# Performance work log

Measured on AMD Instinct MI355X. Metric: run time of the kernel, lower is better.

## Reference

```python
import jax, jax.numpy as jnp
import numpy as np
from jax import lax

DT = 0.1


def setup_inputs() -> dict:
    key = jax.random.key(0)
    k1, k2, k3, k4 = jax.random.split(key, 4)
    Bsz, L, D, N, O = 32, 2048, 256, 64, 256
    x = jax.random.normal(k1, (Bsz, L, D), dtype=jnp.float32)
    # Shift A by 3*I so Re(eig(A)) > 0 -> bilinear-discretized A_tilde is stable
    A = jax.random.uniform(k2, (N, N), dtype=jnp.float32) + 3.0 * jnp.eye(N, dtype=jnp.float32)
    B = jax.random.uniform(k3, (N, D), dtype=jnp.float32)
    C = jax.random.uniform(k4, (O, N), dtype=jnp.float32)
    return {"x": x, "A": A, "B": B, "C": C}


def _s4_forward(x, A, B, C):
    N = A.shape[0]
    I = jnp.eye(N, dtype=A.dtype)
    # Bilinear discretization (as written in the torch source)
    tmp_inv = jnp.linalg.inv(I + A * (DT / 2))
    A_tilde = tmp_inv @ (I - A * (DT / 2))          # [N, N]
    B_tilde = (tmp_inv @ B) * DT                    # [N, D]

    L = x.shape[1]

    # K[i] = C @ A_tilde^i @ B_tilde; carry M = A_tilde^i @ B_tilde
    def step(M, _):
        return A_tilde @ M, C @ M                    # emit [O, D]

    _, K = lax.scan(step, B_tilde, None, length=L)   # K: [L, O, D]

    n = 2 * L - 1  # length after torch's F.pad(x, (0,0,0,L-1))
    x_fft = jnp.fft.rfft(x, n=n, axis=1)             # [B, F, D] complex
    K_fft = jnp.fft.rfft(K, n=n, axis=0)             # [F, O, D] complex
    y_fft = jnp.einsum('bfi,foi->bfo', x_fft, K_fft)
    y = jnp.fft.irfft(y_fft, n=n, axis=1)[:, :L]     # [B, L, O]
    return y


def reference(x, A, B, C):
    return _s4_forward(x, A, B, C)
```

## Files before the change

### kernel.cpp

```cpp
#include <hip/hip_runtime.h>

#define B_SZ   32
#define LEN    2048
#define DIM    256
#define NST    64
#define OUTD   256
#define CHUNK  64
#define NCHUNK (LEN / CHUNK)
#define ROWS   (B_SZ * LEN)

#define OFF_AT   0
#define OFF_A64  4096
#define OFF_CP   8192
#define OFF_S    24576
#define OFF_INST 90112
#define OFF_V    155648
#define OFF_H    OFF_V
#define WS_FLOATS (OFF_V + (size_t)ROWS * 64)

__device__ __forceinline__ void gload16(const float* gp, float* lds_base,
                                        int lane_off_f) {
#if __has_builtin(__builtin_amdgcn_global_load_lds)
  (void)lane_off_f;
  __builtin_amdgcn_global_load_lds(
      (const __attribute__((address_space(1))) unsigned int*)gp,
      (__attribute__((address_space(3))) unsigned int*)lds_base, 16, 0, 0);
#else
  float4 tmp = *(const float4*)gp;
  *(float4*)(lds_base + lane_off_f) = tmp;
#endif
}

__device__ __forceinline__ void mm64(float* dst, const float* a, const float* b,
                                     int t) {
  const int r0 = 4 * (t >> 4), c0 = 4 * (t & 15);
  float acc[4][4] = {};
  for (int k = 0; k < 64; ++k) {
    float4 bv = *(const float4*)(b + k * 68 + c0);
    for (int i = 0; i < 4; ++i) {
      float av = a[(r0 + i) * 68 + k];
      acc[i][0] = fmaf(av, bv.x, acc[i][0]);
      acc[i][1] = fmaf(av, bv.y, acc[i][1]);
      acc[i][2] = fmaf(av, bv.z, acc[i][2]);
      acc[i][3] = fmaf(av, bv.w, acc[i][3]);
    }
  }
  for (int i = 0; i < 4; ++i)
    *(float4*)(dst + (r0 + i) * 68 + c0) =
        make_float4(acc[i][0], acc[i][1], acc[i][2], acc[i][3]);
  __syncthreads();
}

__global__ __launch_bounds__(256) void k_fused0(const float* __restrict__ A,
                                                const float* __restrict__ Bm,
                                                const float* __restrict__ Cm,
                                                const float* __restrict__ x,
                                                float* __restrict__ ws) {
  __shared__ __align__(16) float sh[13056];
  const int t = threadIdx.x;

  if (blockIdx.x == 0) {
    float* Pa = sh;
    float* Pb = sh + 4352;
    float* Pc = sh + 8704;
    float* rbM = Pc;
    float* rbI = Pc + 128;
    float* cb  = Pc + 256;

    const int tc = t & 63;
    const int tr = t >> 6;
    float M[16], Iv[16];
    for (int i = 0; i < 16; ++i) {
      int r = 16 * tr + i;
      M[i] = 0.05f * A[r * 64 + tc] + (r == tc ? 1.0f : 0.0f);
      Iv[i] = (r == tc) ? 1.0f : 0.0f;
    }
    if (tr == 0) { rbM[tc] = M[0]; rbI[tc] = Iv[0]; }
    if (tc == 0)
      for (int i = 0; i < 16; ++i) cb[16 * tr + i] = M[i];
    __syncthreads();

#pragma unroll
    for (int k = 0; k < 64; ++k) {
      const int cur = (k & 1) * 64, nxt = ((k + 1) & 1) * 64;
      float rinv = 1.0f / rbM[cur + k];
      float rM = rbM[cur + tc] * rinv;
      float rI = rbI[cur + tc] * rinv;
#pragma unroll
      for (int i = 0; i < 16; ++i) {
        int r = 16 * tr + i;
        if (r == k) { M[i] = rM; Iv[i] = rI; }
        else {
          float f = cb[cur + r];
          M[i] = fmaf(-f, rM, M[i]);
          Iv[i] = fmaf(-f, rI, Iv[i]);
        }
      }
      if (k < 63) {
        if (tr == ((k + 1) >> 4)) {
          rbM[nxt + tc] = M[(k + 1) & 15];
          rbI[nxt + tc] = Iv[(k + 1) & 15];
        }
        if (tc == k + 1)
          for (int i = 0; i < 16; ++i) cb[nxt + 16 * tr + i] = M[i];
      }
      __syncthreads();
    }

    for (int i = 0; i < 16; ++i) {
      int r = 16 * tr + i;
      float at = 2.0f * Iv[i] - (r == tc ? 1.0f : 0.0f);
      ws[OFF_AT + r * 64 + tc] = at;
      Pa[r * 68 + tc] = at;
      Pc[r * 68 + tc] = Iv[i];
    }
    __syncthreads();

    mm64(Pb, Pa, Pa, t);
    mm64(Pa, Pb, Pb, t);
    mm64(Pb, Pa, Pa, t);
    mm64(Pa, Pb, Pb, t);
    mm64(Pb, Pa, Pa, t);
    mm64(Pa, Pb, Pb, t);
    for (int i = 0; i < 16; ++i) {
      int r = 16 * tr + i;
      ws[OFF_A64 + r * 64 + tc] = Pa[r * 68 + tc];
    }

    {
      const float* Crow = Cm + (size_t)t * 64;
      float4 acc4[16];
      for (int q = 0; q < 16; ++q) acc4[q] = make_float4(0.f, 0.f, 0.f, 0.f);
      for (int k = 0; k < 64; k += 4) {
        float4 c4 = *(const float4*)(Crow + k);
        float ck[4] = {c4.x, c4.y, c4.z, c4.w};
#pragma unroll
        for (int kk = 0; kk < 4; ++kk) {
          const float* mrow = Pc + (k + kk) * 68;
          float c = ck[kk];
#pragma unroll
          for (int q = 0; q < 16; ++q) {
            float4 mv = *(const float4*)(mrow + 4 * q);
            acc4[q].x = fmaf(c, mv.x, acc4[q].x);
            acc4[q].y = fmaf(c, mv.y, acc4[q].y);
            acc4[q].z = fmaf(c, mv.z, acc4[q].z);
            acc4[q].w = fmaf(c, mv.w, acc4[q].w);
          }
        }
      }
      float* cp = ws + OFF_CP + (size_t)t * 64;
      for (int q = 0; q < 16; ++q)
        *(float4*)(cp + 4 * q) =
            make_float4(0.1f * acc4[q].x, 0.1f * acc4[q].y, 0.1f * acc4[q].z,
                        0.1f * acc4[q].w);
    }
  } else {
    float* xs0 = sh;
    float* xs1 = sh + 4096;
    float* bs0 = sh + 8192;
    float* bs1 = sh + 10240;
    const int w = t >> 6, lane = t & 63;
    const int ro8 = lane >> 3, kq8 = lane & 7;
    const int rowbase = ((int)blockIdx.x - 1) * 128;

    auto stage = [&](int d0, float* xbuf, float* bbuf) {
#pragma unroll
      for (int c = 0; c < 4; ++c) {
        int q = 4 * w + c;
        const float* gp = x + (size_t)(rowbase + 8 * q + ro8) * 256 + d0 +
                          4 * (kq8 ^ (q & 7));
        gload16(gp, xbuf + q * 256, lane * 4);
      }
#pragma unroll
      for (int c = 0; c < 2; ++c) {
        int q = 2 * w + c;
        const float* gp =
            Bm + (size_t)(8 * q + ro8) * 256 + d0 + 4 * (kq8 ^ q);
        gload16(gp, bbuf + q * 256, lane * 4);
      }
    };

    stage(0, xs0, bs0);
    const int g = lane >> 4, lm = lane & 15;
    const int r0 = 32 * w + 8 * g, m0 = 4 * lm;
    const int ka = 4 * ((4 * w + g) & 7);
    const int kb = 4 * ((lm >> 1) & 7);
    float acc[8][4] = {};
    float* xc = xs0; float* xn = xs1; float* bc = bs0; float* bn = bs1;
    __syncthreads();

    for (int s = 0; s < 8; ++s) {
      if (s < 7) stage((s + 1) * 32, xn, bn);
      const float* xa = xc + r0 * 32;
      const float* bb = bc + m0 * 32;
#pragma unroll
      for (int k0 = 0; k0 < 32; k0 += 4) {
        float4 a4[8], b4[4];
#pragma unroll
        for (int i = 0; i < 8; ++i)
          a4[i] = *(const float4*)(xa + i * 32 + (k0 ^ ka));
#pragma unroll
        for (int j = 0; j < 4; ++j)
          b4[j] = *(const float4*)(bb + j * 32 + (k0 ^ kb));
#pragma unroll
        for (int i = 0; i < 8; ++i)
#pragma unroll
          for (int j = 0; j < 4; ++j) {
            acc[i][j] = fmaf(a4[i].x, b4[j].x, acc[i][j]);
            acc[i][j] = fmaf(a4[i].y, b4[j].y, acc[i][j]);
            acc[i][j] = fmaf(a4[i].z, b4[j].z, acc[i][j]);
            acc[i][j] = fmaf(a4[i].w, b4[j].w, acc[i][j]);
          }
      }
      __syncthreads();
      float* tp;
      tp = xc; xc = xn; xn = tp;
      tp = bc; bc = bn; bn = tp;
    }
    float* v = ws + OFF_V;
#pragma unroll
    for (int i = 0; i < 8; ++i)
      *(float4*)(v + (size_t)(rowbase + r0 + i) * 64 + m0) =
          make_float4(acc[i][0], acc[i][1], acc[i][2], acc[i][3]);
  }
}

__device__ __forceinline__ void load_areg(const float* __restrict__ M, int r,
                                          int q, float areg[16]) {
  const float4* ap = (const float4*)(M + r * 64 + q * 16);
  float4 a0 = ap[0], a1 = ap[1], a2 = ap[2], a3 = ap[3];
  areg[0] = a0.x; areg[1] = a0.y; areg[2] = a0.z; areg[3] = a0.w;
  areg[4] = a1.x; areg[5] = a1.y; areg[6] = a1.z; areg[7] = a1.w;
  areg[8] = a2.x; areg[9] = a2.y; areg[10] = a2.z; areg[11] = a2.w;
  areg[12] = a3.x; areg[13] = a3.y; areg[14] = a3.z; areg[15] = a3.w;
}

__device__ __forceinline__ float matvec_step(const float areg[16],
                                             const float* __restrict__ hcur,
                                             float* __restrict__ part, int r,
                                             int q, int t) {
  float4 ha = *(const float4*)(hcur + q * 16);
  float4 hb = *(const float4*)(hcur + q * 16 + 4);
  float4 hc = *(const float4*)(hcur + q * 16 + 8);
  float4 hd = *(const float4*)(hcur + q * 16 + 12);
  float p0 = fmaf(areg[0], ha.x, fmaf(areg[4], hb.x, fmaf(areg[8], hc.x, areg[12] * hd.x)));
  float p1 = fmaf(areg[1], ha.y, fmaf(areg[5], hb.y, fmaf(areg[9], hc.y, areg[13] * hd.y)));
  float p2 = fmaf(areg[2], ha.z, fmaf(areg[6], hb.z, fmaf(areg[10], hc.z, areg[14] * hd.z)));
  float p3 = fmaf(areg[3], ha.w, fmaf(areg[7], hb.w, fmaf(areg[11], hc.w, areg[15] * hd.w)));
  part[q * 68 + r] = (p0 + p1) + (p2 + p3);
  __syncthreads();
  float s = 0.0f;
  if (t < 64) s = part[t] + part[68 + t] + part[136 + t] + part[204 + t];
  return s;
}

__global__ __launch_bounds__(256) void k_chunk(float* __restrict__ ws, int phase) {
  __shared__ __align__(16) float hcur[64];
  __shared__ __align__(16) float part[4 * 68];
  __shared__ __align__(16) float ulds[CHUNK * 64];
  const int t = threadIdx.x;
  const int c = blockIdx.x, b = blockIdx.y;
  const int r = t & 63, q = t >> 6;
  float areg[16];
  load_areg(ws + OFF_AT, r, q, areg);
  const float* u = ws + OFF_V + (size_t)(b * LEN + c * CHUNK) * 64;
  for (int i = 0; i < 4; ++i) {
    int e = 4 * (t + 256 * i);
    *(float4*)(ulds + e) = *(const float4*)(u + e);
  }
  if (t < 64)
    hcur[t] = (phase == 3) ? ws[OFF_INST + (b * NCHUNK + c) * 64 + t] : 0.0f;
  __syncthreads();
  for (int st = 0; st < CHUNK; ++st) {
    float s = matvec_step(areg, hcur, part, r, q, t);
    if (t < 64) {
      float hn = s + ulds[st * 64 + t];
      hcur[t] = hn;
      if (phase == 3)
        ws[OFF_H + (size_t)(b * LEN + c * CHUNK + st) * 64 + t] = hn;
      else if (st == CHUNK - 1)
        ws[OFF_S + (b * NCHUNK + c) * 64 + t] = hn;
    }
    __syncthreads();
  }
}

__global__ __launch_bounds__(256) void k_carry(float* __restrict__ ws) {
  __shared__ __align__(16) float hcur[64];
  __shared__ __align__(16) float part[4 * 68];
  __shared__ __align__(16) float slds[NCHUNK * 64];
  const int t = threadIdx.x;
  const int b = blockIdx.x;
  const int r = t & 63, q = t >> 6;
  float areg[16];
  load_areg(ws + OFF_A64, r, q, areg);
  for (int i = 0; i < 2; ++i) {
    int e = 4 * (t + 256 * i);
    *(float4*)(slds + e) = *(const float4*)(ws + OFF_S + b * NCHUNK * 64 + e);
  }
  if (t < 64) {
    hcur[t] = 0.0f;
    ws[OFF_INST + (b * NCHUNK) * 64 + t] = 0.0f;
  }
  __syncthreads();
  for (int c = 1; c < NCHUNK; ++c) {
    float s = matvec_step(areg, hcur, part, r, q, t);
    if (t < 64) {
      float hn = s + slds[(c - 1) * 64 + t];
      hcur[t] = hn;
      ws[OFF_INST + (b * NCHUNK + c) * 64 + t] = hn;
    }
    __syncthreads();
  }
}

__global__ __launch_bounds__(256) void k_ygemm(const float* __restrict__ ws,
                                               float* __restrict__ y) {
  __shared__ __align__(16) float sh[16384];
  float* hs = sh;
  float* cs = sh + 8192;
  const int t = threadIdx.x;
  const int w = t >> 6, lane = t & 63;
  const int rowbase = blockIdx.x * 128;
  const int obase = blockIdx.y * 128;
  const float* H = ws + OFF_H;
  const float* CP = ws + OFF_CP;

  const int ro4 = lane >> 4, kq16 = lane & 15;
#pragma unroll
  for (int c = 0; c < 8; ++c) {
    int q = 8 * w + c;
    int row = 4 * q + ro4;
    int sd = 4 * (kq16 ^ ((row >> 3) & 7));
    gload16(H + (size_t)(rowbase + row) * 64 + sd, hs + q * 256, lane * 4);
    gload16(CP + (size_t)(obase + row) * 64 + sd, cs + q * 256, lane * 4);
  }
  __syncthreads();

  const int g = lane >> 4, lm = lane & 15;
  const int r0 = 32 * w + 8 * g, o0 = 8 * lm;
  const int ka = 4 * ((4 * w + g) & 7);
  const int kb = 4 * (lm & 7);
  const float* ha = hs + r0 * 64;
  const float* cbp = cs + o0 * 64;
  float acc[8][8] = {};
#pragma unroll
  for (int k0 = 0; k0 < 64; k0 += 4) {
    float4 a4[8], b4[8];
#pragma unroll
    for (int i = 0; i < 8; ++i)
      a4[i] = *(const float4*)(ha + i * 64 + (k0 ^ ka));
#pragma unroll
    for (int j = 0; j < 8; ++j)
      b4[j] = *(const float4*)(cbp + j * 64 + (k0 ^ kb));
#pragma unroll
    for (int i = 0; i < 8; ++i)
#pragma unroll
      for (int j = 0; j < 8; ++j) {
        acc[i][j] = fmaf(a4[i].x, b4[j].x, acc[i][j]);
        acc[i][j] = fmaf(a4[i].y, b4[j].y, acc[i][j]);
        acc[i][j] = fmaf(a4[i].z, b4[j].z, acc[i][j]);
        acc[i][j] = fmaf(a4[i].w, b4[j].w, acc[i][j]);
      }
  }
#pragma unroll
  for (int i = 0; i < 8; ++i) {
    float* yp = y + (size_t)(rowbase + r0 + i) * 256 + obase + o0;
    *(float4*)(yp) = make_float4(acc[i][0], acc[i][1], acc[i][2], acc[i][3]);
    *(float4*)(yp + 4) = make_float4(acc[i][4], acc[i][5], acc[i][6], acc[i][7]);
  }
}

extern "C" void kernel_launch(void* const* d_in, const int* in_sizes, int n_in,
                              void* d_out, int out_size, void* d_ws,
                              size_t ws_size, hipStream_t stream) {
  const float* x = (const float*)d_in[0];
  const float* A = (const float*)d_in[1];
  const float* Bm = (const float*)d_in[2];
  const float* Cm = (const float*)d_in[3];
  float* y = (float*)d_out;
  float* ws = (float*)d_ws;
  if (ws_size < (size_t)WS_FLOATS * sizeof(float)) return;

  hipLaunchKernelGGL(k_fused0, dim3(1 + ROWS / 128), dim3(256), 0, stream, A,
                     Bm, Cm, x, ws);
  hipLaunchKernelGGL(k_chunk, dim3(NCHUNK, B_SZ), dim3(256), 0, stream, ws, 1);
  hipLaunchKernelGGL(k_carry, dim3(B_SZ), dim3(256), 0, stream, ws);
  hipLaunchKernelGGL(k_chunk, dim3(NCHUNK, B_SZ), dim3(256), 0, stream, ws, 3);
  hipLaunchKernelGGL(k_ygemm, dim3(ROWS / 128, OUTD / 128), dim3(256), 0,
                     stream, ws, y);
}
```

Baseline: 260.3 us.

## Fuse y GEMM into chunk scan, one-wave-per-chunk recurrences, register-resident x GEMM

Replaces the four-wave matvec recurrence, which needed block-wide barriers every step, with one wavefront per chunk holding a full row of A_tilde in registers. The output GEMM against C' is fused into the second chunk pass, so the H state is never written to or re-read from global memory. The x·B GEMM now streams x directly into registers with B staged in LDS. The A^64 power and C' products move into extra blocks of the first chunk pass. Trade-offs: 64-float register arrays per thread, a large LDS footprint that limits occupancy, and dependence on the ordering of launches within one stream.

```diff
diff --git a/kernel.cpp b/kernel.cpp
--- a/kernel.cpp
+++ b/kernel.cpp
@@ -10,13 +10,15 @@
 #define ROWS   (B_SZ * LEN)
 
 #define OFF_AT   0
-#define OFF_A64  4096
-#define OFF_CP   8192
-#define OFF_S    24576
-#define OFF_INST 90112
-#define OFF_V    155648
-#define OFF_H    OFF_V
+#define OFF_P64  4096
+#define OFF_MINV 8192
+#define OFF_CP   12288
+#define OFF_S    28672
+#define OFF_INST 94208
+#define OFF_V    159744
 #define WS_FLOATS (OFF_V + (size_t)ROWS * 64)
+
+#define KEYR(row) ((((row) >> 3) ^ (row)) & 7)
 
 __device__ __forceinline__ void gload16(const float* gp, float* lds_base,
                                         int lane_off_f) {
@@ -37,6 +39,7 @@
   float acc[4][4] = {};
   for (int k = 0; k < 64; ++k) {
     float4 bv = *(const float4*)(b + k * 68 + c0);
+#pragma unroll
     for (int i = 0; i < 4; ++i) {
       float av = a[(r0 + i) * 68 + k];
       acc[i][0] = fmaf(av, bv.x, acc[i][0]);
@@ -45,6 +48,8 @@
       acc[i][3] = fmaf(av, bv.w, acc[i][3]);
     }
   }
+  __syncthreads();
+#pragma unroll
   for (int i = 0; i < 4; ++i)
     *(float4*)(dst + (r0 + i) * 68 + c0) =
         make_float4(acc[i][0], acc[i][1], acc[i][2], acc[i][3]);
@@ -53,23 +58,19 @@
 
 __global__ __launch_bounds__(256) void k_fused0(const float* __restrict__ A,
                                                 const float* __restrict__ Bm,
-                                                const float* __restrict__ Cm,
                                                 const float* __restrict__ x,
                                                 float* __restrict__ ws) {
-  __shared__ __align__(16) float sh[13056];
+  __shared__ __align__(16) float sh[16384];
   const int t = threadIdx.x;
 
   if (blockIdx.x == 0) {
-    float* Pa = sh;
-    float* Pb = sh + 4352;
-    float* Pc = sh + 8704;
-    float* rbM = Pc;
-    float* rbI = Pc + 128;
-    float* cb  = Pc + 256;
-
+    float* rbM = sh;
+    float* rbI = sh + 128;
+    float* cb  = sh + 256;
     const int tc = t & 63;
     const int tr = t >> 6;
     float M[16], Iv[16];
+#pragma unroll
     for (int i = 0; i < 16; ++i) {
       int r = 16 * tr + i;
       M[i] = 0.05f * A[r * 64 + tc] + (r == tc ? 1.0f : 0.0f);
@@ -79,7 +80,6 @@
     if (tc == 0)
       for (int i = 0; i < 16; ++i) cb[16 * tr + i] = M[i];
     __syncthreads();
-
 #pragma unroll
     for (int k = 0; k < 64; ++k) {
       const int cur = (k & 1) * 64, nxt = ((k + 1) & 1) * 64;
@@ -106,268 +106,297 @@
       }
       __syncthreads();
     }
-
+#pragma unroll
     for (int i = 0; i < 16; ++i) {
       int r = 16 * tr + i;
-      float at = 2.0f * Iv[i] - (r == tc ? 1.0f : 0.0f);
-      ws[OFF_AT + r * 64 + tc] = at;
-      Pa[r * 68 + tc] = at;
-      Pc[r * 68 + tc] = Iv[i];
+      ws[OFF_AT + r * 64 + tc] = 2.0f * Iv[i] - (r == tc ? 1.0f : 0.0f);
+      ws[OFF_MINV + r * 64 + tc] = Iv[i];
+    }
+  } else {
+    float* Bl = sh;
+    const int w = t >> 6, lane = t & 63;
+#pragma unroll
+    for (int c2 = 0; c2 < 16; ++c2) {
+      int m = 16 * w + c2;
+      const float* gp = Bm + (size_t)m * 256 + 4 * (lane ^ ((m >> 2) & 7));
+      gload16(gp, Bl + m * 256, lane * 4);
     }
     __syncthreads();
 
-    mm64(Pb, Pa, Pa, t);
-    mm64(Pa, Pb, Pb, t);
-    mm64(Pb, Pa, Pa, t);
-    mm64(Pa, Pb, Pb, t);
-    mm64(Pb, Pa, Pa, t);
-    mm64(Pa, Pb, Pb, t);
-    for (int i = 0; i < 16; ++i) {
-      int r = 16 * tr + i;
-      ws[OFF_A64 + r * 64 + tc] = Pa[r * 68 + tc];
-    }
-
-    {
-      const float* Crow = Cm + (size_t)t * 64;
-      float4 acc4[16];
-      for (int q = 0; q < 16; ++q) acc4[q] = make_float4(0.f, 0.f, 0.f, 0.f);
-      for (int k = 0; k < 64; k += 4) {
-        float4 c4 = *(const float4*)(Crow + k);
-        float ck[4] = {c4.x, c4.y, c4.z, c4.w};
-#pragma unroll
-        for (int kk = 0; kk < 4; ++kk) {
-          const float* mrow = Pc + (k + kk) * 68;
-          float c = ck[kk];
-#pragma unroll
-          for (int q = 0; q < 16; ++q) {
-            float4 mv = *(const float4*)(mrow + 4 * q);
-            acc4[q].x = fmaf(c, mv.x, acc4[q].x);
-            acc4[q].y = fmaf(c, mv.y, acc4[q].y);
-            acc4[q].z = fmaf(c, mv.z, acc4[q].z);
-            acc4[q].w = fmaf(c, mv.w, acc4[q].w);
+    const int band = w >> 1, half = w & 1;
+    const int rg = lane >> 3, mg = lane & 7;
+    const int rowbase = ((int)blockIdx.x - 1) * 128 + band * 64;
+    const int m0 = half * 32 + mg * 4;
+    const float* xw = x + (size_t)rowbase * 256;
+
+    float acc[8][4] = {};
+    float4 aA[8], aB[8];
+#pragma unroll
+    for (int i = 0; i < 8; ++i)
+      aA[i] = *(const float4*)(xw + (size_t)(rg + 8 * i) * 256);
+
+    for (int k0 = 0; k0 < 256; k0 += 8) {
+#pragma unroll
+      for (int i = 0; i < 8; ++i)
+        aB[i] = *(const float4*)(xw + (size_t)(rg + 8 * i) * 256 + k0 + 4);
+      {
+        const int bq = 4 * ((k0 >> 2) ^ mg);
+        float4 b4[4];
+#pragma unroll
+        for (int j = 0; j < 4; ++j)
+          b4[j] = *(const float4*)(Bl + (m0 + j) * 256 + bq);
+#pragma unroll
+        for (int i = 0; i < 8; ++i)
+#pragma unroll
+          for (int j = 0; j < 4; ++j) {
+            acc[i][j] = fmaf(aA[i].x, b4[j].x, acc[i][j]);
+            acc[i][j] = fmaf(aA[i].y, b4[j].y, acc[i][j]);
+            acc[i][j] = fmaf(aA[i].z, b4[j].z, acc[i][j]);
+            acc[i][j] = fmaf(aA[i].w, b4[j].w, acc[i][j]);
+          }
+      }
+      if (k0 + 8 < 256) {
+#pragma unroll
+        for (int i = 0; i < 8; ++i)
+          aA[i] = *(const float4*)(xw + (size_t)(rg + 8 * i) * 256 + k0 + 8);
+      }
+      {
+        const int bq = 4 * (((k0 + 4) >> 2) ^ mg);
+        float4 b4[4];
+#pragma unroll
+        for (int j = 0; j < 4; ++j)
+          b4[j] = *(const float4*)(Bl + (m0 + j) * 256 + bq);
+#pragma unroll
+        for (int i = 0; i < 8; ++i)
+#pragma unroll
+          for (int j = 0; j < 4; ++j) {
+            acc[i][j] = fmaf(aB[i].x, b4[j].x, acc[i][j]);
+            acc[i][j] = fmaf(aB[i].y, b4[j].y, acc[i][j]);
+            acc[i][j] = fmaf(aB[i].z, b4[j].z, acc[i][j]);
+            acc[i][j] = fmaf(aB[i].w, b4[j].w, acc[i][j]);
+          }
+      }
+    }
+    float* v = ws + OFF_V;
+#pragma unroll
+    for (int i = 0; i < 8; ++i)
+      *(float4*)(v + (size_t)(rowbase + rg + 8 * i) * 64 + m0) =
+          make_float4(acc[i][0], acc[i][1], acc[i][2], acc[i][3]);
+  }
+}
+
+__global__ __launch_bounds__(256) void k_chunk(float* __restrict__ ws,
+                                               const float* __restrict__ Cm,
+                                               float* __restrict__ y,
+                                               int phase) {
+  __shared__ __align__(16) float sh[33024];
+  float* Hs  = sh;
+  float* CPs = sh + 16384;
+  float* hb  = sh + 32768;
+  const int t = threadIdx.x, w = t >> 6, lane = t & 63;
+
+  if (blockIdx.x == 8) {
+    if (blockIdx.y == 0) {
+      float* Pa = sh;
+      float* Pb = sh + 4352;
+#pragma unroll
+      for (int i = 0; i < 4; ++i) {
+        int e = 4 * (t + 256 * i);
+        int r = e >> 6, c2 = e & 63;
+        *(float4*)(Pa + r * 68 + c2) = *(const float4*)(ws + OFF_AT + e);
+      }
+      __syncthreads();
+      mm64(Pb, Pa, Pa, t);
+      mm64(Pa, Pb, Pb, t);
+      mm64(Pb, Pa, Pa, t);
+      mm64(Pa, Pb, Pb, t);
+      mm64(Pb, Pa, Pa, t);
+      mm64(Pa, Pb, Pb, t);
+#pragma unroll
+      for (int i = 0; i < 4; ++i) {
+        int e = 4 * (t + 256 * i);
+        int r = e >> 6, c2 = e & 63;
+        *(float4*)(ws + OFF_P64 + e) = *(const float4*)(Pa + r * 68 + c2);
+      }
+    } else if (blockIdx.y == 1) {
+      float* Ms = sh;
+      float* Cs = sh + 4352;
+#pragma unroll
+      for (int i = 0; i < 4; ++i) {
+        int e = 4 * (t + 256 * i);
+        int kk = e >> 6, nn = e & 63;
+        *(float4*)(Ms + kk * 68 + nn) = *(const float4*)(ws + OFF_MINV + e);
+      }
+      __syncthreads();
+      const int r0 = 4 * (t >> 4), c0 = 4 * (t & 15);
+      for (int ob = 0; ob < 4; ++ob) {
+#pragma unroll
+        for (int i = 0; i < 4; ++i) {
+          int e = 4 * (t + 256 * i);
+          int orow = e >> 6, kk = e & 63;
+          *(float4*)(Cs + orow * 68 + kk) =
+              *(const float4*)(Cm + (size_t)(64 * ob + orow) * 64 + kk);
+        }
+        __syncthreads();
+        float acc[4][4] = {};
+        for (int k = 0; k < 64; ++k) {
+          float4 bv = *(const float4*)(Ms + k * 68 + c0);
+#pragma unroll
+          for (int i = 0; i < 4; ++i) {
+            float av = Cs[(r0 + i) * 68 + k];
+            acc[i][0] = fmaf(av, bv.x, acc[i][0]);
+            acc[i][1] = fmaf(av, bv.y, acc[i][1]);
+            acc[i][2] = fmaf(av, bv.z, acc[i][2]);
+            acc[i][3] = fmaf(av, bv.w, acc[i][3]);
           }
         }
-      }
-      float* cp = ws + OFF_CP + (size_t)t * 64;
-      for (int q = 0; q < 16; ++q)
-        *(float4*)(cp + 4 * q) =
-            make_float4(0.1f * acc4[q].x, 0.1f * acc4[q].y, 0.1f * acc4[q].z,
-                        0.1f * acc4[q].w);
-    }
-  } else {
-    float* xs0 = sh;
-    float* xs1 = sh + 4096;
-    float* bs0 = sh + 8192;
-    float* bs1 = sh + 10240;
-    const int w = t >> 6, lane = t & 63;
-    const int ro8 = lane >> 3, kq8 = lane & 7;
-    const int rowbase = ((int)blockIdx.x - 1) * 128;
-
-    auto stage = [&](int d0, float* xbuf, float* bbuf) {
-#pragma unroll
-      for (int c = 0; c < 4; ++c) {
-        int q = 4 * w + c;
-        const float* gp = x + (size_t)(rowbase + 8 * q + ro8) * 256 + d0 +
-                          4 * (kq8 ^ (q & 7));
-        gload16(gp, xbuf + q * 256, lane * 4);
-      }
-#pragma unroll
-      for (int c = 0; c < 2; ++c) {
-        int q = 2 * w + c;
-        const float* gp =
-            Bm + (size_t)(8 * q + ro8) * 256 + d0 + 4 * (kq8 ^ q);
-        gload16(gp, bbuf + q * 256, lane * 4);
-      }
-    };
-
-    stage(0, xs0, bs0);
-    const int g = lane >> 4, lm = lane & 15;
-    const int r0 = 32 * w + 8 * g, m0 = 4 * lm;
-    const int ka = 4 * ((4 * w + g) & 7);
-    const int kb = 4 * ((lm >> 1) & 7);
-    float acc[8][4] = {};
-    float* xc = xs0; float* xn = xs1; float* bc = bs0; float* bn = bs1;
-    __syncthreads();
-
-    for (int s = 0; s < 8; ++s) {
-      if (s < 7) stage((s + 1) * 32, xn, bn);
-      const float* xa = xc + r0 * 32;
-      const float* bb = bc + m0 * 32;
-#pragma unroll
-      for (int k0 = 0; k0 < 32; k0 += 4) {
-        float4 a4[8], b4[4];
-#pragma unroll
-        for (int i = 0; i < 8; ++i)
-          a4[i] = *(const float4*)(xa + i * 32 + (k0 ^ ka));
-#pragma unroll
-        for (int j = 0; j < 4; ++j)
-          b4[j] = *(const float4*)(bb + j * 32 + (k0 ^ kb));
-#pragma unroll
-        for (int i = 0; i < 8; ++i)
-#pragma unroll
-          for (int j = 0; j < 4; ++j) {
-            acc[i][j] = fmaf(a4[i].x, b4[j].x, acc[i][j]);
-            acc[i][j] = fmaf(a4[i].y, b4[j].y, acc[i][j]);
-            acc[i][j] = fmaf(a4[i].z, b4[j].z, acc[i][j]);
-            acc[i][j] = fmaf(a4[i].w, b4[j].w, acc[i][j]);
-          }
-      }
-      __syncthreads();
-      float* tp;
-      tp = xc; xc = xn; xn = tp;
-      tp = bc; bc = bn; bn = tp;
-    }
-    float* v = ws + OFF_V;
-#pragma unroll
-    for (int i = 0; i < 8; ++i)
-      *(float4*)(v + (size_t)(rowbase + r0 + i) * 64 + m0) =
+#pragma unroll
+        for (int i = 0; i < 4; ++i)
+          *(float4*)(ws + OFF_CP + (size_t)(64 * ob + r0 + i) * 64 + c0) =
+              make_float4(0.1f * acc[i][0], 0.1f * acc[i][1], 0.1f * acc[i][2],
+                          0.1f * acc[i][3]);
+        __syncthreads();
+      }
+    }
+    return;
+  }
+
+  const int b = blockIdx.y, c = blockIdx.x * 4 + w;
+  const int r = lane;
+
+  float a[64];
+#pragma unroll
+  for (int k4 = 0; k4 < 16; ++k4) {
+    float4 v4 = *(const float4*)(ws + OFF_AT + r * 64 + 4 * k4);
+    a[4 * k4 + 0] = v4.x; a[4 * k4 + 1] = v4.y;
+    a[4 * k4 + 2] = v4.z; a[4 * k4 + 3] = v4.w;
+  }
+
+  float* Hw = Hs + w * 4096;
+  const float* u = ws + OFF_V + (size_t)(b * LEN + c * CHUNK) * 64;
+#pragma unroll
+  for (int q = 0; q < 16; ++q) {
+    int trow = 4 * q + (lane >> 4);
+    int s4 = lane & 15;
+    gload16(u + trow * 64 + 4 * (s4 ^ KEYR(trow)), Hw + q * 256, lane * 4);
+  }
+  if (phase == 3) {
+#pragma unroll
+    for (int q = 0; q < 16; ++q) {
+      int qq = 16 * w + q;
+      int orow = 4 * qq + (lane >> 4);
+      int s4 = lane & 15;
+      gload16(ws + OFF_CP + (size_t)orow * 64 + 4 * (s4 ^ KEYR(orow)),
+              CPs + qq * 256, lane * 4);
+    }
+  }
+  float h0 = (phase == 3)
+                 ? ws[OFF_INST + (size_t)(b * NCHUNK + c) * 64 + r]
+                 : 0.0f;
+  asm volatile("s_waitcnt vmcnt(0)" ::: "memory");
+  float* hw = hb + w * 64;
+  hw[r] = h0;
+  asm volatile("" ::: "memory");
+
+  float hlast = h0;
+  for (int tt = 0; tt < 64; ++tt) {
+    float ac0 = 0.f, ac1 = 0.f, ac2 = 0.f, ac3 = 0.f;
+#pragma unroll
+    for (int k = 0; k < 64; k += 4) {
+      float4 hv = *(const float4*)(hw + k);
+      ac0 = fmaf(a[k + 0], hv.x, ac0);
+      ac1 = fmaf(a[k + 1], hv.y, ac1);
+      ac2 = fmaf(a[k + 2], hv.z, ac2);
+      ac3 = fmaf(a[k + 3], hv.w, ac3);
+    }
+    const int slot = tt * 64 + 4 * ((r >> 2) ^ KEYR(tt)) + (r & 3);
+    float hn = ((ac0 + ac1) + (ac2 + ac3)) + Hw[slot];
+    hw[r] = hn;
+    if (phase == 3) Hw[slot] = hn;
+    hlast = hn;
+    asm volatile("" ::: "memory");
+  }
+
+  if (phase != 3) {
+    ws[OFF_S + (size_t)(b * NCHUNK + c) * 64 + r] = hlast;
+    return;
+  }
+
+  __syncthreads();
+  const int rg = lane >> 3, og = lane & 7;
+  for (int p = 0; p < 4; ++p) {
+    float acc[8][8] = {};
+    for (int k0 = 0; k0 < 64; k0 += 4) {
+      float4 a4[8], b4[8];
+#pragma unroll
+      for (int i = 0; i < 8; ++i) {
+        int trow = rg + 8 * i;
+        a4[i] = *(const float4*)(Hw + trow * 64 + 4 * ((k0 >> 2) ^ KEYR(trow)));
+      }
+#pragma unroll
+      for (int j = 0; j < 8; ++j) {
+        int orow = p * 64 + og * 8 + j;
+        b4[j] =
+            *(const float4*)(CPs + orow * 64 + 4 * ((k0 >> 2) ^ KEYR(orow)));
+      }
+#pragma unroll
+      for (int i = 0; i < 8; ++i)
+#pragma unroll
+        for (int j = 0; j < 8; ++j) {
+          acc[i][j] = fmaf(a4[i].x, b4[j].x, acc[i][j]);
+          acc[i][j] = fmaf(a4[i].y, b4[j].y, acc[i][j]);
+          acc[i][j] = fmaf(a4[i].z, b4[j].z, acc[i][j]);
+          acc[i][j] = fmaf(a4[i].w, b4[j].w, acc[i][j]);
+        }
+    }
+#pragma unroll
+    for (int i = 0; i < 8; ++i) {
+      float* yp = y + (size_t)(b * LEN + c * CHUNK + rg + 8 * i) * 256 +
+                  p * 64 + og * 8;
+      *(float4*)(yp) =
           make_float4(acc[i][0], acc[i][1], acc[i][2], acc[i][3]);
-  }
-}
-
-__device__ __forceinline__ void load_areg(const float* __restrict__ M, int r,
-                                          int q, float areg[16]) {
-  const float4* ap = (const float4*)(M + r * 64 + q * 16);
-  float4 a0 = ap[0], a1 = ap[1], a2 = ap[2], a3 = ap[3];
-  areg[0] = a0.x; areg[1] = a0.y; areg[2] = a0.z; areg[3] = a0.w;
-  areg[4] = a1.x; areg[5] = a1.y; areg[6] = a1.z; areg[7] = a1.w;
-  areg[8] = a2.x; areg[9] = a2.y; areg[10] = a2.z; areg[11] = a2.w;
-  areg[12] = a3.x; areg[13] = a3.y; areg[14] = a3.z; areg[15] = a3.w;
-}
-
-__device__ __forceinline__ float matvec_step(const float areg[16],
-                                             const float* __restrict__ hcur,
-                                             float* __restrict__ part, int r,
-                                             int q, int t) {
-  float4 ha = *(const float4*)(hcur + q * 16);
-  float4 hb = *(const float4*)(hcur + q * 16 + 4);
-  float4 hc = *(const float4*)(hcur + q * 16 + 8);
-  float4 hd = *(const float4*)(hcur + q * 16 + 12);
-  float p0 = fmaf(areg[0], ha.x, fmaf(areg[4], hb.x, fmaf(areg[8], hc.x, areg[12] * hd.x)));
-  float p1 = fmaf(areg[1], ha.y, fmaf(areg[5], hb.y, fmaf(areg[9], hc.y, areg[13] * hd.y)));
-  float p2 = fmaf(areg[2], ha.z, fmaf(areg[6], hb.z, fmaf(areg[10], hc.z, areg[14] * hd.z)));
-  float p3 = fmaf(areg[3], ha.w, fmaf(areg[7], hb.w, fmaf(areg[11], hc.w, areg[15] * hd.w)));
-  part[q * 68 + r] = (p0 + p1) + (p2 + p3);
-  __syncthreads();
-  float s = 0.0f;
-  if (t < 64) s = part[t] + part[68 + t] + part[136 + t] + part[204 + t];
-  return s;
-}
-
-__global__ __launch_bounds__(256) void k_chunk(float* __restrict__ ws, int phase) {
-  __shared__ __align__(16) float hcur[64];
-  __shared__ __align__(16) float part[4 * 68];
-  __shared__ __align__(16) float ulds[CHUNK * 64];
-  const int t = threadIdx.x;
-  const int c = blockIdx.x, b = blockIdx.y;
-  const int r = t & 63, q = t >> 6;
-  float areg[16];
-  load_areg(ws + OFF_AT, r, q, areg);
-  const float* u = ws + OFF_V + (size_t)(b * LEN + c * CHUNK) * 64;
-  for (int i = 0; i < 4; ++i) {
-    int e = 4 * (t + 256 * i);
-    *(float4*)(ulds + e) = *(const float4*)(u + e);
-  }
-  if (t < 64)
-    hcur[t] = (phase == 3) ? ws[OFF_INST + (b * NCHUNK + c) * 64 + t] : 0.0f;
-  __syncthreads();
-  for (int st = 0; st < CHUNK; ++st) {
-    float s = matvec_step(areg, hcur, part, r, q, t);
-    if (t < 64) {
-      float hn = s + ulds[st * 64 + t];
-      hcur[t] = hn;
-      if (phase == 3)
-        ws[OFF_H + (size_t)(b * LEN + c * CHUNK + st) * 64 + t] = hn;
-      else if (st == CHUNK - 1)
-        ws[OFF_S + (b * NCHUNK + c) * 64 + t] = hn;
-    }
-    __syncthreads();
+      *(float4*)(yp + 4) =
+          make_float4(acc[i][4], acc[i][5], acc[i][6], acc[i][7]);
+    }
   }
 }
 
 __global__ __launch_bounds__(256) void k_carry(float* __restrict__ ws) {
-  __shared__ __align__(16) float hcur[64];
-  __shared__ __align__(16) float part[4 * 68];
-  __shared__ __align__(16) float slds[NCHUNK * 64];
-  const int t = threadIdx.x;
-  const int b = blockIdx.x;
-  const int r = t & 63, q = t >> 6;
-  float areg[16];
-  load_areg(ws + OFF_A64, r, q, areg);
-  for (int i = 0; i < 2; ++i) {
-    int e = 4 * (t + 256 * i);
-    *(float4*)(slds + e) = *(const float4*)(ws + OFF_S + b * NCHUNK * 64 + e);
-  }
-  if (t < 64) {
-    hcur[t] = 0.0f;
-    ws[OFF_INST + (b * NCHUNK) * 64 + t] = 0.0f;
-  }
-  __syncthreads();
-  for (int c = 1; c < NCHUNK; ++c) {
-    float s = matvec_step(areg, hcur, part, r, q, t);
-    if (t < 64) {
-      float hn = s + slds[(c - 1) * 64 + t];
-      hcur[t] = hn;
-      ws[OFF_INST + (b * NCHUNK + c) * 64 + t] = hn;
-    }
-    __syncthreads();
-  }
-}
-
-__global__ __launch_bounds__(256) void k_ygemm(const float* __restrict__ ws,
-                                               float* __restrict__ y) {
-  __shared__ __align__(16) float sh[16384];
-  float* hs = sh;
-  float* cs = sh + 8192;
-  const int t = threadIdx.x;
-  const int w = t >> 6, lane = t & 63;
-  const int rowbase = blockIdx.x * 128;
-  const int obase = blockIdx.y * 128;
-  const float* H = ws + OFF_H;
-  const float* CP = ws + OFF_CP;
-
-  const int ro4 = lane >> 4, kq16 = lane & 15;
-#pragma unroll
-  for (int c = 0; c < 8; ++c) {
-    int q = 8 * w + c;
-    int row = 4 * q + ro4;
-    int sd = 4 * (kq16 ^ ((row >> 3) & 7));
-    gload16(H + (size_t)(rowbase + row) * 64 + sd, hs + q * 256, lane * 4);
-    gload16(CP + (size_t)(obase + row) * 64 + sd, cs + q * 256, lane * 4);
-  }
-  __syncthreads();
-
-  const int g = lane >> 4, lm = lane & 15;
-  const int r0 = 32 * w + 8 * g, o0 = 8 * lm;
-  const int ka = 4 * ((4 * w + g) & 7);
-  const int kb = 4 * (lm & 7);
-  const float* ha = hs + r0 * 64;
-  const float* cbp = cs + o0 * 64;
-  float acc[8][8] = {};
-#pragma unroll
-  for (int k0 = 0; k0 < 64; k0 += 4) {
-    float4 a4[8], b4[8];
-#pragma unroll
-    for (int i = 0; i < 8; ++i)
-      a4[i] = *(const float4*)(ha + i * 64 + (k0 ^ ka));
-#pragma unroll
-    for (int j = 0; j < 8; ++j)
-      b4[j] = *(const float4*)(cbp + j * 64 + (k0 ^ kb));
-#pragma unroll
-    for (int i = 0; i < 8; ++i)
-#pragma unroll
-      for (int j = 0; j < 8; ++j) {
-        acc[i][j] = fmaf(a4[i].x, b4[j].x, acc[i][j]);
-        acc[i][j] = fmaf(a4[i].y, b4[j].y, acc[i][j]);
-        acc[i][j] = fmaf(a4[i].z, b4[j].z, acc[i][j]);
-        acc[i][j] = fmaf(a4[i].w, b4[j].w, acc[i][j]);
-      }
-  }
-#pragma unroll
-  for (int i = 0; i < 8; ++i) {
-    float* yp = y + (size_t)(rowbase + r0 + i) * 256 + obase + o0;
-    *(float4*)(yp) = make_float4(acc[i][0], acc[i][1], acc[i][2], acc[i][3]);
-    *(float4*)(yp + 4) = make_float4(acc[i][4], acc[i][5], acc[i][6], acc[i][7]);
+  __shared__ __align__(16) float slds[4][NCHUNK * 64];
+  __shared__ __align__(16) float hbc[4][64];
+  const int t = threadIdx.x, w = t >> 6, lane = t & 63;
+  const int b = blockIdx.x * 4 + w;
+  const int r = lane;
+  float a[64];
+#pragma unroll
+  for (int k4 = 0; k4 < 16; ++k4) {
+    float4 v4 = *(const float4*)(ws + OFF_P64 + r * 64 + 4 * k4);
+    a[4 * k4 + 0] = v4.x; a[4 * k4 + 1] = v4.y;
+    a[4 * k4 + 2] = v4.z; a[4 * k4 + 3] = v4.w;
+  }
+#pragma unroll
+  for (int q = 0; q < 8; ++q)
+    gload16(ws + OFF_S + (size_t)b * (NCHUNK * 64) + q * 256 + 4 * lane,
+            &slds[w][q * 256], lane * 4);
+  ws[OFF_INST + (size_t)b * (NCHUNK * 64) + r] = 0.0f;
+  asm volatile("s_waitcnt vmcnt(0)" ::: "memory");
+  float* hw = hbc[w];
+  hw[r] = 0.0f;
+  asm volatile("" ::: "memory");
+  for (int cc = 1; cc < NCHUNK; ++cc) {
+    float ac0 = 0.f, ac1 = 0.f, ac2 = 0.f, ac3 = 0.f;
+#pragma unroll
+    for (int k = 0; k < 64; k += 4) {
+      float4 hv = *(const float4*)(hw + k);
+      ac0 = fmaf(a[k + 0], hv.x, ac0);
+      ac1 = fmaf(a[k + 1], hv.y, ac1);
+      ac2 = fmaf(a[k + 2], hv.z, ac2);
+      ac3 = fmaf(a[k + 3], hv.w, ac3);
+    }
+    float hn = ((ac0 + ac1) + (ac2 + ac3)) + slds[w][(cc - 1) * 64 + r];
+    hw[r] = hn;
+    ws[OFF_INST + (size_t)b * (NCHUNK * 64) + cc * 64 + r] = hn;
+    asm volatile("" ::: "memory");
   }
 }
 
@@ -383,10 +412,10 @@
   if (ws_size < (size_t)WS_FLOATS * sizeof(float)) return;
 
   hipLaunchKernelGGL(k_fused0, dim3(1 + ROWS / 128), dim3(256), 0, stream, A,
-                     Bm, Cm, x, ws);
-  hipLaunchKernelGGL(k_chunk, dim3(NCHUNK, B_SZ), dim3(256), 0, stream, ws, 1);
-  hipLaunchKernelGGL(k_carry, dim3(B_SZ), dim3(256), 0, stream, ws);
-  hipLaunchKernelGGL(k_chunk, dim3(NCHUNK, B_SZ), dim3(256), 0, stream, ws, 3);
-  hipLaunchKernelGGL(k_ygemm, dim3(ROWS / 128, OUTD / 128), dim3(256), 0,
-                     stream, ws, y);
-}
+                     Bm, x, ws);
+  hipLaunchKernelGGL(k_chunk, dim3(NCHUNK / 4 + 1, B_SZ), dim3(256), 0, stream,
+                     ws, Cm, y, 1);
+  hipLaunchKernelGGL(k_carry, dim3(B_SZ / 4), dim3(256), 0, stream, ws);
+  hipLaunchKernelGGL(k_chunk, dim3(NCHUNK / 4, B_SZ), dim3(256), 0, stream, ws,
+                     Cm, y, 3);
+}
```

Measured after the change: 285.6 us. +9.7%, slower.
